# Optimization experiments

Hardware: AMD Instinct MI355X
Metric: run time of the kernel (lower is better)

Reference implementation:

```python
import jax, jax.numpy as jnp
import numpy as np

H = 128  # hidden_size
I = 28   # input_size
C = 10   # num_classes


def setup_inputs() -> dict:
    key = jax.random.key(0)
    ks = jax.random.split(key, 11)
    s = 1.0 / np.sqrt(H)  # torch nn.RNN init scale
    return {
        "x": jax.random.normal(ks[0], (8192, 28, I), dtype=jnp.float32),
        "W_ih0": jax.random.uniform(ks[1], (H, I), jnp.float32, -s, s),
        "W_hh0": jax.random.uniform(ks[2], (H, H), jnp.float32, -s, s),
        "b_ih0": jax.random.uniform(ks[3], (H,), jnp.float32, -s, s),
        "b_hh0": jax.random.uniform(ks[4], (H,), jnp.float32, -s, s),
        "W_ih1": jax.random.uniform(ks[5], (H, H), jnp.float32, -s, s),
        "W_hh1": jax.random.uniform(ks[6], (H, H), jnp.float32, -s, s),
        "b_ih1": jax.random.uniform(ks[7], (H,), jnp.float32, -s, s),
        "b_hh1": jax.random.uniform(ks[8], (H,), jnp.float32, -s, s),
        "fc_w": jax.random.uniform(ks[9], (C, H), jnp.float32, -s, s),
        "fc_b": jax.random.uniform(ks[10], (C,), jnp.float32, -s, s),
    }


def _rnn_layer_full(x, W_ih, b_ih, W_hh, b_hh):
    # x: [B, T, D] -> full output sequence [B, T, H]
    B = x.shape[0]
    h0 = jnp.zeros((B, H), x.dtype)
    xw = jnp.einsum('btd,hd->bth', x, W_ih) + b_ih  # precompute input GEMM

    def step(h, xw_t):
        h = jnp.tanh(xw_t + h @ W_hh.T + b_hh)
        return h, h

    _, ys = jax.lax.scan(step, h0, jnp.swapaxes(xw, 0, 1))  # [T, B, H]
    return jnp.swapaxes(ys, 0, 1)


def _rnn_layer_last(x, W_ih, b_ih, W_hh, b_hh):
    # only the final hidden state is needed downstream
    B = x.shape[0]
    h0 = jnp.zeros((B, H), x.dtype)
    xw = jnp.einsum('btd,hd->bth', x, W_ih) + b_ih

    def step(h, xw_t):
        h = jnp.tanh(xw_t + h @ W_hh.T + b_hh)
        return h, None

    h_last, _ = jax.lax.scan(step, h0, jnp.swapaxes(xw, 0, 1))
    return h_last


def reference(x, W_ih0, W_hh0, b_ih0, b_hh0, W_ih1, W_hh1, b_ih1, b_hh1, fc_w, fc_b):
    out0 = _rnn_layer_full(x, W_ih0, b_ih0, W_hh0, b_hh0)   # [B, T, H]
    h_last = _rnn_layer_last(out0, W_ih1, b_ih1, W_hh1, b_hh1)  # [B, H] == out[:, -1, :]
    return h_last @ fc_w.T + fc_b  # [B, C]
```

## Files before the change

### kernel.cpp

```cpp
#include <hip/hip_runtime.h>

#define HSZ 128
#define ISZ 28
#define TSZ 28
#define CSZ 10
#define BT  16
#define NT  512
#define HP  136
#define XP  40

typedef _Float16 half_t;
typedef _Float16 v8h __attribute__((ext_vector_type(8)));
typedef _Float16 v4h __attribute__((ext_vector_type(4)));
typedef float v4f __attribute__((ext_vector_type(4)));

__device__ __forceinline__ float fast_tanh(float x) {
    float e = __expf(2.f * x);
    return 1.f - 2.f * __builtin_amdgcn_rcpf(e + 1.f);
}

__global__ __launch_bounds__(NT, 4)
void rnn_mfma5(const float* __restrict__ x,
               const float* __restrict__ W_ih0, const float* __restrict__ W_hh0,
               const float* __restrict__ b_ih0, const float* __restrict__ b_hh0,
               const float* __restrict__ W_ih1, const float* __restrict__ W_hh1,
               const float* __restrict__ b_ih1, const float* __restrict__ b_hh1,
               const float* __restrict__ fc_w, const float* __restrict__ fc_b,
               float* __restrict__ out)
{
    __shared__ half_t h0s[2][BT * HP];
    __shared__ half_t h1s[2][BT * HP];
    __shared__ half_t xss[2][BT * XP];

    const int tid  = threadIdx.x;
    const int wave = tid >> 6;
    const int lane = tid & 63;
    const int ln   = lane & 15;
    const int quad = lane >> 4;
    const int kq   = quad * 8;
    const int b0   = blockIdx.x * BT;
    const int base = wave * 16;
    const int row  = base + ln;

    v8h aWx, aW0[4], aW1i[4], aW1h[4];
    v4f bias0, bias1;
    {
        float4 p = *(const float4*)(b_ih0 + base + quad * 4);
        float4 q = *(const float4*)(b_hh0 + base + quad * 4);
        bias0 = (v4f){p.x + q.x, p.y + q.y, p.z + q.z, p.w + q.w};
        p = *(const float4*)(b_ih1 + base + quad * 4);
        q = *(const float4*)(b_hh1 + base + quad * 4);
        bias1 = (v4f){p.x + q.x, p.y + q.y, p.z + q.z, p.w + q.w};
    }
    {
        const float* pw = W_ih0 + row * ISZ + kq;
        float4 a = *(const float4*)pw;
        float4 b = (kq < 24) ? *(const float4*)(pw + 4) : make_float4(0.f, 0.f, 0.f, 0.f);
        aWx = (v8h){(half_t)a.x, (half_t)a.y, (half_t)a.z, (half_t)a.w,
                    (half_t)(kq + 4 < ISZ ? b.x : 0.f), (half_t)(kq + 5 < ISZ ? b.y : 0.f),
                    (half_t)(kq + 6 < ISZ ? b.z : 0.f), (half_t)(kq + 7 < ISZ ? b.w : 0.f)};
    }
#pragma unroll
    for (int ks = 0; ks < 4; ++ks) {
        const float4* p0 = (const float4*)(W_hh0 + row * HSZ + ks * 32 + kq);
        const float4* p1 = (const float4*)(W_ih1 + row * HSZ + ks * 32 + kq);
        const float4* p2 = (const float4*)(W_hh1 + row * HSZ + ks * 32 + kq);
        float4 a = p0[0], b = p0[1];
        aW0[ks] = (v8h){(half_t)a.x, (half_t)a.y, (half_t)a.z, (half_t)a.w,
                        (half_t)b.x, (half_t)b.y, (half_t)b.z, (half_t)b.w};
        a = p1[0]; b = p1[1];
        aW1i[ks] = (v8h){(half_t)a.x, (half_t)a.y, (half_t)a.z, (half_t)a.w,
                         (half_t)b.x, (half_t)b.y, (half_t)b.z, (half_t)b.w};
        a = p2[0]; b = p2[1];
        aW1h[ks] = (v8h){(half_t)a.x, (half_t)a.y, (half_t)a.z, (half_t)a.w,
                         (half_t)b.x, (half_t)b.y, (half_t)b.z, (half_t)b.w};
    }

    const int xm = tid >> 5;
    const int xi = tid & 31;
    const int xiC = xi < ISZ ? xi : ISZ - 1;
    const float* xrow = x + (size_t)(b0 + xm) * (TSZ * ISZ) + xiC;

    xss[0][xm * XP + xi] = (half_t)xrow[0];
    xss[1][xm * XP + xi] = (half_t)xrow[ISZ];
    float xc = xrow[2 * ISZ];

    for (int idx = tid; idx < BT * HP; idx += NT)
        h1s[0][idx] = (half_t)0.f;
    __syncthreads();

    {
        const v8h bx = *(const v8h*)&xss[0][ln * XP + kq];
        v4f a0 = bias0;
        a0 = __builtin_amdgcn_mfma_f32_16x16x32_f16(aWx, bx, a0, 0, 0, 0);
        v4h p = {(half_t)fast_tanh(a0[0]), (half_t)fast_tanh(a0[1]),
                 (half_t)fast_tanh(a0[2]), (half_t)fast_tanh(a0[3])};
        *(v4h*)&h0s[0][ln * HP + base + quad * 4] = p;
    }
    __syncthreads();

    auto seg = [&](int t, int pr, bool doX) __attribute__((always_inline)) {
        int tn = t + 3; if (tn > TSZ - 1) tn = TSZ - 1;
        const float xn = xrow[tn * ISZ];

        v8h bh0_0 = *(const v8h*)&h0s[pr][ln * HP + 0 * 32 + kq];
        v8h bh0_1 = *(const v8h*)&h0s[pr][ln * HP + 1 * 32 + kq];
        v8h bh0_2 = *(const v8h*)&h0s[pr][ln * HP + 2 * 32 + kq];
        v8h bh0_3 = *(const v8h*)&h0s[pr][ln * HP + 3 * 32 + kq];
        const v8h bx = *(const v8h*)&xss[pr ^ 1][ln * XP + kq];

        v4f c0 = bias0, d0 = (v4f){0.f, 0.f, 0.f, 0.f};
        v4f c1 = bias1, d1 = (v4f){0.f, 0.f, 0.f, 0.f};

        c0 = __builtin_amdgcn_mfma_f32_16x16x32_f16(aWx,      bx,    c0, 0, 0, 0);
        c1 = __builtin_amdgcn_mfma_f32_16x16x32_f16(aW1i[0],  bh0_0, c1, 0, 0, 0);
        v8h bh1_0 = *(const v8h*)&h1s[pr][ln * HP + 0 * 32 + kq];
        d1 = __builtin_amdgcn_mfma_f32_16x16x32_f16(aW1h[0],  bh1_0, d1, 0, 0, 0);
        c0 = __builtin_amdgcn_mfma_f32_16x16x32_f16(aW0[0],   bh0_0, c0, 0, 0, 0);
        d0 = __builtin_amdgcn_mfma_f32_16x16x32_f16(aW0[1],   bh0_1, d0, 0, 0, 0);
        c1 = __builtin_amdgcn_mfma_f32_16x16x32_f16(aW1i[1],  bh0_1, c1, 0, 0, 0);
        v8h bh1_1 = *(const v8h*)&h1s[pr][ln * HP + 1 * 32 + kq];
        d1 = __builtin_amdgcn_mfma_f32_16x16x32_f16(aW1h[1],  bh1_1, d1, 0, 0, 0);
        c0 = __builtin_amdgcn_mfma_f32_16x16x32_f16(aW0[2],   bh0_2, c0, 0, 0, 0);
        d0 = __builtin_amdgcn_mfma_f32_16x16x32_f16(aW0[3],   bh0_3, d0, 0, 0, 0);
        c1 = __builtin_amdgcn_mfma_f32_16x16x32_f16(aW1i[2],  bh0_2, c1, 0, 0, 0);
        v8h bh1_2 = *(const v8h*)&h1s[pr][ln * HP + 2 * 32 + kq];
        d1 = __builtin_amdgcn_mfma_f32_16x16x32_f16(aW1h[2],  bh1_2, d1, 0, 0, 0);
        c1 = __builtin_amdgcn_mfma_f32_16x16x32_f16(aW1i[3],  bh0_3, c1, 0, 0, 0);
        v8h bh1_3 = *(const v8h*)&h1s[pr][ln * HP + 3 * 32 + kq];
        d1 = __builtin_amdgcn_mfma_f32_16x16x32_f16(aW1h[3],  bh1_3, d1, 0, 0, 0);

        const v4f a0 = c0 + d0;
        const v4f a1 = c1 + d1;

        v4h p1 = {(half_t)fast_tanh(a1[0]), (half_t)fast_tanh(a1[1]),
                  (half_t)fast_tanh(a1[2]), (half_t)fast_tanh(a1[3])};
        *(v4h*)&h1s[pr ^ 1][ln * HP + base + quad * 4] = p1;
        v4h p0 = {(half_t)fast_tanh(a0[0]), (half_t)fast_tanh(a0[1]),
                  (half_t)fast_tanh(a0[2]), (half_t)fast_tanh(a0[3])};
        *(v4h*)&h0s[pr ^ 1][ln * HP + base + quad * 4] = p0;

        if (doX)
            xss[pr][xm * XP + xi] = (half_t)xc;
        xc = xn;

        __syncthreads();
    };

    for (int tp = 0; tp < 13; ++tp) {
        seg(2 * tp,     0, true);
        seg(2 * tp + 1, 1, true);
    }
    seg(26, 0, false);

    {
        v4f c1 = bias1, d1 = (v4f){0.f, 0.f, 0.f, 0.f};
#pragma unroll
        for (int ks = 0; ks < 4; ++ks) {
            const v8h bh0 = *(const v8h*)&h0s[1][ln * HP + ks * 32 + kq];
            const v8h bh1 = *(const v8h*)&h1s[1][ln * HP + ks * 32 + kq];
            c1 = __builtin_amdgcn_mfma_f32_16x16x32_f16(aW1i[ks], bh0, c1, 0, 0, 0);
            d1 = __builtin_amdgcn_mfma_f32_16x16x32_f16(aW1h[ks], bh1, d1, 0, 0, 0);
        }
        const v4f a1 = c1 + d1;
        v4h p1 = {(half_t)fast_tanh(a1[0]), (half_t)fast_tanh(a1[1]),
                  (half_t)fast_tanh(a1[2]), (half_t)fast_tanh(a1[3])};
        *(v4h*)&h1s[0][ln * HP + base + quad * 4] = p1;
    }
    __syncthreads();

    if (tid < BT * CSZ) {
        const int m = tid / CSZ, cc = tid - m * CSZ;
        float s = fc_b[cc];
#pragma unroll
        for (int k8 = 0; k8 < HSZ / 8; ++k8) {
            const v8h hv = *(const v8h*)&h1s[0][m * HP + k8 * 8];
            const float4 w0 = *(const float4*)(fc_w + cc * HSZ + k8 * 8);
            const float4 w1 = *(const float4*)(fc_w + cc * HSZ + k8 * 8 + 4);
            s += (float)hv[0] * w0.x + (float)hv[1] * w0.y +
                 (float)hv[2] * w0.z + (float)hv[3] * w0.w +
                 (float)hv[4] * w1.x + (float)hv[5] * w1.y +
                 (float)hv[6] * w1.z + (float)hv[7] * w1.w;
        }
        out[(b0 + m) * CSZ + cc] = s;
    }
}

extern "C" void kernel_launch(void* const* d_in, const int* in_sizes, int n_in,
                              void* d_out, int out_size, void* d_ws, size_t ws_size,
                              hipStream_t stream) {
    const float* x     = (const float*)d_in[0];
    const float* W_ih0 = (const float*)d_in[1];
    const float* W_hh0 = (const float*)d_in[2];
    const float* b_ih0 = (const float*)d_in[3];
    const float* b_hh0 = (const float*)d_in[4];
    const float* W_ih1 = (const float*)d_in[5];
    const float* W_hh1 = (const float*)d_in[6];
    const float* b_ih1 = (const float*)d_in[7];
    const float* b_hh1 = (const float*)d_in[8];
    const float* fc_w  = (const float*)d_in[9];
    const float* fc_b  = (const float*)d_in[10];
    float* out = (float*)d_out;

    const int B = in_sizes[0] / (TSZ * ISZ);
    dim3 grid(B / BT), block(NT);
    rnn_mfma5<<<grid, block, 0, stream>>>(x, W_ih0, W_hh0, b_ih0, b_hh0,
                                          W_ih1, W_hh1, b_ih1, b_hh1,
                                          fc_w, fc_b, out);
}
```

Baseline: 128.4 us.

## Pack tanh via cvt_pkrtz, schedule MFMA/LDS interleave, stagger block starts

Computes tanh with a direct exp2 and packs fp16 pairs with cvt_pkrtz. All LDS reads for a step are hoisted ahead of the MFMA chain, and sched_group_barrier hints interleave the reads with the MFMAs. Every other group of 256 blocks sleeps briefly after loading weights, to stagger phases and spread out contention on global memory and barriers. The changes are independent micro-optimizations. The sleep costs idle cycles, and round-to-zero conversion slightly changes numerics.

Result: no change. 127.7 us (-0.6%).

```diff
diff --git a/kernel.cpp b/kernel.cpp
--- a/kernel.cpp
+++ b/kernel.cpp
@@ -12,15 +12,27 @@
 typedef _Float16 half_t;
 typedef _Float16 v8h __attribute__((ext_vector_type(8)));
 typedef _Float16 v4h __attribute__((ext_vector_type(4)));
+typedef _Float16 v2h __attribute__((ext_vector_type(2)));
+typedef __fp16   v2fp16 __attribute__((ext_vector_type(2)));
 typedef float v4f __attribute__((ext_vector_type(4)));
 
+#define MFMA16(A, B, C) __builtin_amdgcn_mfma_f32_16x16x32_f16((A), (B), (C), 0, 0, 0)
+
 __device__ __forceinline__ float fast_tanh(float x) {
-    float e = __expf(2.f * x);
+    float e = __builtin_amdgcn_exp2f(x * 2.8853900817779268f);
     return 1.f - 2.f * __builtin_amdgcn_rcpf(e + 1.f);
 }
 
+__device__ __forceinline__ v4h pack4(const v4f a) {
+    v2fp16 lo = __builtin_amdgcn_cvt_pkrtz(fast_tanh(a[0]), fast_tanh(a[1]));
+    v2fp16 hi = __builtin_amdgcn_cvt_pkrtz(fast_tanh(a[2]), fast_tanh(a[3]));
+    v2h lo2 = __builtin_bit_cast(v2h, lo);
+    v2h hi2 = __builtin_bit_cast(v2h, hi);
+    return (v4h){lo2[0], lo2[1], hi2[0], hi2[1]};
+}
+
 __global__ __launch_bounds__(NT, 4)
-void rnn_mfma5(const float* __restrict__ x,
+void rnn_mfma6(const float* __restrict__ x,
                const float* __restrict__ W_ih0, const float* __restrict__ W_hh0,
                const float* __restrict__ b_ih0, const float* __restrict__ b_hh0,
                const float* __restrict__ W_ih1, const float* __restrict__ W_hh1,
@@ -76,6 +88,11 @@
                          (half_t)b.x, (half_t)b.y, (half_t)b.z, (half_t)b.w};
     }
 
+    if ((blockIdx.x >> 8) & 1) {
+        __builtin_amdgcn_s_sleep(8);
+        __builtin_amdgcn_s_sleep(8);
+    }
+
     const int xm = tid >> 5;
     const int xi = tid & 31;
     const int xiC = xi < ISZ ? xi : ISZ - 1;
@@ -91,11 +108,8 @@
 
     {
         const v8h bx = *(const v8h*)&xss[0][ln * XP + kq];
-        v4f a0 = bias0;
-        a0 = __builtin_amdgcn_mfma_f32_16x16x32_f16(aWx, bx, a0, 0, 0, 0);
-        v4h p = {(half_t)fast_tanh(a0[0]), (half_t)fast_tanh(a0[1]),
-                 (half_t)fast_tanh(a0[2]), (half_t)fast_tanh(a0[3])};
-        *(v4h*)&h0s[0][ln * HP + base + quad * 4] = p;
+        v4f a0 = MFMA16(aWx, bx, bias0);
+        *(v4h*)&h0s[0][ln * HP + base + quad * 4] = pack4(a0);
     }
     __syncthreads();
 
@@ -103,42 +117,48 @@
         int tn = t + 3; if (tn > TSZ - 1) tn = TSZ - 1;
         const float xn = xrow[tn * ISZ];
 
-        v8h bh0_0 = *(const v8h*)&h0s[pr][ln * HP + 0 * 32 + kq];
-        v8h bh0_1 = *(const v8h*)&h0s[pr][ln * HP + 1 * 32 + kq];
-        v8h bh0_2 = *(const v8h*)&h0s[pr][ln * HP + 2 * 32 + kq];
-        v8h bh0_3 = *(const v8h*)&h0s[pr][ln * HP + 3 * 32 + kq];
-        const v8h bx = *(const v8h*)&xss[pr ^ 1][ln * XP + kq];
+        const half_t* h0p = &h0s[pr][ln * HP + kq];
+        const half_t* h1p = &h1s[pr][ln * HP + kq];
+
+        const v8h bx    = *(const v8h*)&xss[pr ^ 1][ln * XP + kq];
+        const v8h bh0_0 = *(const v8h*)(h0p + 0 * 32);
+        const v8h bh0_1 = *(const v8h*)(h0p + 1 * 32);
+        const v8h bh1_0 = *(const v8h*)(h1p + 0 * 32);
+        const v8h bh0_2 = *(const v8h*)(h0p + 2 * 32);
+        const v8h bh1_1 = *(const v8h*)(h1p + 1 * 32);
+        const v8h bh0_3 = *(const v8h*)(h0p + 3 * 32);
+        const v8h bh1_2 = *(const v8h*)(h1p + 2 * 32);
+        const v8h bh1_3 = *(const v8h*)(h1p + 3 * 32);
 
         v4f c0 = bias0, d0 = (v4f){0.f, 0.f, 0.f, 0.f};
         v4f c1 = bias1, d1 = (v4f){0.f, 0.f, 0.f, 0.f};
-
-        c0 = __builtin_amdgcn_mfma_f32_16x16x32_f16(aWx,      bx,    c0, 0, 0, 0);
-        c1 = __builtin_amdgcn_mfma_f32_16x16x32_f16(aW1i[0],  bh0_0, c1, 0, 0, 0);
-        v8h bh1_0 = *(const v8h*)&h1s[pr][ln * HP + 0 * 32 + kq];
-        d1 = __builtin_amdgcn_mfma_f32_16x16x32_f16(aW1h[0],  bh1_0, d1, 0, 0, 0);
-        c0 = __builtin_amdgcn_mfma_f32_16x16x32_f16(aW0[0],   bh0_0, c0, 0, 0, 0);
-        d0 = __builtin_amdgcn_mfma_f32_16x16x32_f16(aW0[1],   bh0_1, d0, 0, 0, 0);
-        c1 = __builtin_amdgcn_mfma_f32_16x16x32_f16(aW1i[1],  bh0_1, c1, 0, 0, 0);
-        v8h bh1_1 = *(const v8h*)&h1s[pr][ln * HP + 1 * 32 + kq];
-        d1 = __builtin_amdgcn_mfma_f32_16x16x32_f16(aW1h[1],  bh1_1, d1, 0, 0, 0);
-        c0 = __builtin_amdgcn_mfma_f32_16x16x32_f16(aW0[2],   bh0_2, c0, 0, 0, 0);
-        d0 = __builtin_amdgcn_mfma_f32_16x16x32_f16(aW0[3],   bh0_3, d0, 0, 0, 0);
-        c1 = __builtin_amdgcn_mfma_f32_16x16x32_f16(aW1i[2],  bh0_2, c1, 0, 0, 0);
-        v8h bh1_2 = *(const v8h*)&h1s[pr][ln * HP + 2 * 32 + kq];
-        d1 = __builtin_amdgcn_mfma_f32_16x16x32_f16(aW1h[2],  bh1_2, d1, 0, 0, 0);
-        c1 = __builtin_amdgcn_mfma_f32_16x16x32_f16(aW1i[3],  bh0_3, c1, 0, 0, 0);
-        v8h bh1_3 = *(const v8h*)&h1s[pr][ln * HP + 3 * 32 + kq];
-        d1 = __builtin_amdgcn_mfma_f32_16x16x32_f16(aW1h[3],  bh1_3, d1, 0, 0, 0);
+        c0 = MFMA16(aWx,     bx,    c0);
+        c1 = MFMA16(aW1i[0], bh0_0, c1);
+        c0 = MFMA16(aW0[0],  bh0_0, c0);
+        d0 = MFMA16(aW0[1],  bh0_1, d0);
+        d1 = MFMA16(aW1h[0], bh1_0, d1);
+        c1 = MFMA16(aW1i[1], bh0_1, c1);
+        c0 = MFMA16(aW0[2],  bh0_2, c0);
+        d1 = MFMA16(aW1h[1], bh1_1, d1);
+        c1 = MFMA16(aW1i[2], bh0_2, c1);
+        d0 = MFMA16(aW0[3],  bh0_3, d0);
+        d1 = MFMA16(aW1h[2], bh1_2, d1);
+        c1 = MFMA16(aW1i[3], bh0_3, c1);
+        d1 = MFMA16(aW1h[3], bh1_3, d1);
+
+        __builtin_amdgcn_sched_group_barrier(0x020, 1, 0);
+        __builtin_amdgcn_sched_group_barrier(0x100, 2, 0);
+#pragma unroll
+        for (int i = 0; i < 7; ++i) {
+            __builtin_amdgcn_sched_group_barrier(0x008, 1, 0);
+            __builtin_amdgcn_sched_group_barrier(0x100, 1, 0);
+        }
+        __builtin_amdgcn_sched_group_barrier(0x008, 6, 0);
 
         const v4f a0 = c0 + d0;
         const v4f a1 = c1 + d1;
-
-        v4h p1 = {(half_t)fast_tanh(a1[0]), (half_t)fast_tanh(a1[1]),
-                  (half_t)fast_tanh(a1[2]), (half_t)fast_tanh(a1[3])};
-        *(v4h*)&h1s[pr ^ 1][ln * HP + base + quad * 4] = p1;
-        v4h p0 = {(half_t)fast_tanh(a0[0]), (half_t)fast_tanh(a0[1]),
-                  (half_t)fast_tanh(a0[2]), (half_t)fast_tanh(a0[3])};
-        *(v4h*)&h0s[pr ^ 1][ln * HP + base + quad * 4] = p0;
+        *(v4h*)&h1s[pr ^ 1][ln * HP + base + quad * 4] = pack4(a1);
+        *(v4h*)&h0s[pr ^ 1][ln * HP + base + quad * 4] = pack4(a0);
 
         if (doX)
             xss[pr][xm * XP + xi] = (half_t)xc;
@@ -159,13 +179,11 @@
         for (int ks = 0; ks < 4; ++ks) {
             const v8h bh0 = *(const v8h*)&h0s[1][ln * HP + ks * 32 + kq];
             const v8h bh1 = *(const v8h*)&h1s[1][ln * HP + ks * 32 + kq];
-            c1 = __builtin_amdgcn_mfma_f32_16x16x32_f16(aW1i[ks], bh0, c1, 0, 0, 0);
-            d1 = __builtin_amdgcn_mfma_f32_16x16x32_f16(aW1h[ks], bh1, d1, 0, 0, 0);
+            c1 = MFMA16(aW1i[ks], bh0, c1);
+            d1 = MFMA16(aW1h[ks], bh1, d1);
         }
         const v4f a1 = c1 + d1;
-        v4h p1 = {(half_t)fast_tanh(a1[0]), (half_t)fast_tanh(a1[1]),
-                  (half_t)fast_tanh(a1[2]), (half_t)fast_tanh(a1[3])};
-        *(v4h*)&h1s[0][ln * HP + base + quad * 4] = p1;
+        *(v4h*)&h1s[0][ln * HP + base + quad * 4] = pack4(a1);
     }
     __syncthreads();
 
@@ -204,7 +222,7 @@
 
     const int B = in_sizes[0] / (TSZ * ISZ);
     dim3 grid(B / BT), block(NT);
-    rnn_mfma5<<<grid, block, 0, stream>>>(x, W_ih0, W_hh0, b_ih0, b_hh0,
+    rnn_mfma6<<<grid, block, 0, stream>>>(x, W_ih0, W_hh0, b_ih0, b_hh0,
                                           W_ih1, W_hh1, b_ih1, b_hh1,
                                           fc_w, fc_b, out);
 }
```
